# Kernel tuning notes

Measured on AMD Instinct MI355X. Metric: run time of the kernel, lower is better.

The kernel has to match this reference:

```python
import jax, jax.numpy as jnp
import numpy as np

EPS = 1e-6

def _normalize(x, eps=1e-12):
    n = jnp.linalg.norm(x, axis=-1, keepdims=True)
    return x / jnp.maximum(n, eps)

def _gather_nodes(nodes, idx):
    # nodes [B,N,C], idx [B,N,K] -> [B,N,K,C]
    B = nodes.shape[0]
    return nodes[jnp.arange(B)[:, None, None], idx]

def _dist(X, top_k):
    dX = X[:, None, :, :] - X[:, :, None, :]          # [B,N,N,3]
    D = jnp.sqrt(jnp.sum(dX * dX, axis=-1) + EPS)      # [B,N,N]
    neg_vals, E_idx = jax.lax.top_k(-D, top_k)         # smallest distances
    return D, -neg_vals, E_idx

def _gs_dist(D):
    D_min, D_max, D_count = 0.0, 20.0, 15
    D_mu = jnp.linspace(D_min, D_max, D_count)         # [15]
    D_sigma = (D_max - D_min) / D_count
    return jnp.exp(-(((D[..., None] - D_mu) / D_sigma) ** 2))

def _pos_encodings(E_idx, num_embeddings=16):
    N = E_idx.shape[1]
    ii = jnp.arange(N, dtype=jnp.float32)[None, :, None]
    d = (E_idx.astype(jnp.float32) - ii)[..., None]    # [B,N,K,1]
    freq = jnp.exp(jnp.arange(0, num_embeddings, 2, dtype=jnp.float32)
                   * -(np.log(10000.0) / num_embeddings))  # [8]
    angles = d * freq                                   # [B,N,K,8]
    return jnp.concatenate([jnp.cos(angles), jnp.sin(angles)], axis=-1)

def _orientations_coarse(X, E_idx, eps=1e-6):
    dX = X[:, 1:, :] - X[:, :-1, :]
    U = _normalize(dX)
    u_2, u_1, u_0 = U[:, :-2], U[:, 1:-1], U[:, 2:]
    n_2 = _normalize(jnp.cross(u_2, u_1))
    n_1 = _normalize(jnp.cross(u_1, u_0))
    cosA = jnp.clip(-(u_1 * u_0).sum(-1), -1 + eps, 1 - eps)
    A = jnp.arccos(cosA)
    cosD = jnp.clip((n_2 * n_1).sum(-1), -1 + eps, 1 - eps)
    Dang = jnp.sign((u_2 * n_1).sum(-1)) * jnp.arccos(cosD)
    AD = jnp.stack([jnp.cos(A), jnp.sin(A) * jnp.cos(Dang), jnp.sin(A) * jnp.sin(Dang)], axis=2)
    AD = jnp.pad(AD, ((0, 0), (1, 2), (0, 0)))          # [B,N,3]
    o_1 = _normalize(u_2 - u_1)
    O = jnp.stack([o_1, n_2, jnp.cross(o_1, n_2)], axis=2)  # [B,N-3,3,3]
    O = O.reshape(O.shape[0], O.shape[1], 9)
    O = jnp.pad(O, ((0, 0), (1, 2), (0, 0)))            # [B,N,9]
    O_nb = _gather_nodes(O, E_idx)                      # [B,N,K,9]
    X_nb = _gather_nodes(X, E_idx)                      # [B,N,K,3]
    O3 = O.reshape(O.shape[0], O.shape[1], 3, 3)
    dXn = X_nb - X[:, :, None, :]                       # [B,N,K,3]
    dU = jnp.einsum('bnij,bnkj->bnki', O3, dXn)         # rotate into local frame
    dU = _normalize(dU)
    # NOTE: original also computes R = O^T @ O_nb and quaternions Q, but Q is
    # dead code (never returned); omitted here (jit would DCE it anyway).
    return AD, dU

def setup_inputs() -> dict:
    key = jax.random.key(0)
    coords = jax.random.normal(key, (2, 4096, 3), dtype=jnp.float32) * 10.0
    return {"coords": coords, "num_k": 30}

def reference(coords, num_k):
    D, D_neighbors, E_idx = _dist(coords, num_k)
    gs_d = _gs_dist(D_neighbors)
    pos_emb = _pos_encodings(E_idx)
    AD_features, O_features = _orientations_coarse(coords, E_idx)
    return pos_emb, AD_features, O_features, gs_d, D_neighbors, E_idx
```

## Files before the change

### kernel.cpp

```cpp
#include <hip/hip_runtime.h>
#include <hip/hip_bf16.h>

constexpr int B = 2;
constexpr int N = 4096;
constexpr int K = 30;
constexpr int ROWS_PER_BLK = 4;

constexpr size_t OFF_POS = 0;
constexpr size_t OFF_AD  = OFF_POS + (size_t)B * N * K * 16;
constexpr size_t OFF_O   = OFF_AD  + (size_t)B * N * 3;
constexpr size_t OFF_GS  = OFF_O   + (size_t)B * N * K * 3;
constexpr size_t OFF_DN  = OFF_GS  + (size_t)B * N * K * 15;
constexpr size_t OFF_E   = OFF_DN  + (size_t)B * N * K;

constexpr float BIGD = 1e30f;
constexpr unsigned int BIGJ = 0xFFFFFFFFu;

struct F3 { float x, y, z; };

template <bool ISBF16>
__device__ __forceinline__ float ldx(const void* __restrict__ X, int idx) {
  if constexpr (ISBF16) {
    return __bfloat162float(((const __hip_bfloat16*)X)[idx]);
  } else {
    return ((const float*)X)[idx];
  }
}

template <bool ISBF16>
__device__ __forceinline__ float dist_core(float px, float py, float pz,
                                           float xi, float yi, float zi) {
#pragma clang fp contract(off)
  const float dx = px - xi;
  const float dy = py - yi;
  const float dz = pz - zi;
  return sqrtf(((dx * dx + dy * dy) + dz * dz) + 1e-6f);
}

template <bool ISBF16>
__device__ __forceinline__ float distf(const void* __restrict__ Xb, int j,
                                       float xi, float yi, float zi) {
  float px, py, pz;
  if constexpr (ISBF16) {
    px = ldx<true>(Xb, j * 3 + 0);
    py = ldx<true>(Xb, j * 3 + 1);
    pz = ldx<true>(Xb, j * 3 + 2);
  } else {
    const F3 p = ((const F3*)Xb)[j];
    px = p.x; py = p.y; pz = p.z;
  }
  return dist_core<ISBF16>(px, py, pz, xi, yi, zi);
}

template <int CTRL>
__device__ __forceinline__ float dpp_min_f32(float v) {
  const int mv = __builtin_amdgcn_update_dpp(__float_as_int(BIGD), __float_as_int(v),
                                             CTRL, 0xF, 0xF, false);
  return fminf(__int_as_float(mv), v);
}
template <int CTRL>
__device__ __forceinline__ unsigned int dpp_min_u32(unsigned int v) {
  const unsigned int mv = (unsigned int)__builtin_amdgcn_update_dpp(
      (int)BIGJ, (int)v, CTRL, 0xF, 0xF, false);
  return mv < v ? mv : v;
}
__device__ __forceinline__ float wave_min_f32_bcast(float v) {
  v = dpp_min_f32<0x111>(v);
  v = dpp_min_f32<0x112>(v);
  v = dpp_min_f32<0x114>(v);
  v = dpp_min_f32<0x118>(v);
  v = dpp_min_f32<0x142>(v);
  v = dpp_min_f32<0x143>(v);
  return __int_as_float(__builtin_amdgcn_readlane(__float_as_int(v), 63));
}
__device__ __forceinline__ unsigned int wave_min_u32_bcast(unsigned int v) {
  v = dpp_min_u32<0x111>(v);
  v = dpp_min_u32<0x112>(v);
  v = dpp_min_u32<0x114>(v);
  v = dpp_min_u32<0x118>(v);
  v = dpp_min_u32<0x142>(v);
  v = dpp_min_u32<0x143>(v);
  return (unsigned int)__builtin_amdgcn_readlane((int)v, 63);
}

__device__ __forceinline__ void lex_argmin(float d0, int j0,
                                           float& dmin, unsigned int& jmin) {
  dmin = wave_min_f32_bcast(d0);
  const unsigned long long tie = __ballot(d0 == dmin);
  if (__popcll(tie) == 1) {
    const int wl = __ffsll((unsigned long long)tie) - 1;
    jmin = (unsigned int)__builtin_amdgcn_readlane(j0, wl);
  } else {
    const unsigned int jc = (d0 == dmin) ? (unsigned int)j0 : BIGJ;
    jmin = wave_min_u32_bcast(jc);
  }
}

__device__ __forceinline__ float red2pi(float x) {
  return x - 6.28318530718f * rintf(x * 0.15915494309f);
}

__device__ __forceinline__ void norm3(float& x, float& y, float& z) {
  float n = sqrtf((x * x + y * y) + z * z);
  n = fmaxf(n, 1e-12f);
  x /= n; y /= n; z /= n;
}

__device__ __forceinline__ void cross3(float ax, float ay, float az,
                                       float bx, float by, float bz,
                                       float& cx, float& cy, float& cz) {
  cx = ay * bz - az * by;
  cy = az * bx - ax * bz;
  cz = ax * by - ay * bx;
}

template <bool ISBF16>
__device__ __forceinline__ void body(const void* __restrict__ Xb,
                                     float* __restrict__ out,
                                     int b, int i, int lane) {
  const float xi = ldx<ISBF16>(Xb, i * 3 + 0);
  const float yi = ldx<ISBF16>(Xb, i * 3 + 1);
  const float zi = ldx<ISBF16>(Xb, i * 3 + 2);

  float d0 = BIGD, d1 = BIGD;
  int   j0 = 0x7FFFFFFF, j1 = 0x7FFFFFFF;
  if constexpr (!ISBF16) {
    const F3* __restrict__ P = ((const F3*)Xb) + lane;
#pragma unroll 8
    for (int t = 0; t < 64; ++t) {
      const F3 p = P[t * 64];
      const int j = t * 64 + lane;
      const float d = dist_core<ISBF16>(p.x, p.y, p.z, xi, yi, zi);
      const bool lt1 = d < d1;
      const float td = lt1 ? d : d1;
      const int   tj = lt1 ? j : j1;
      const bool lt0 = td < d0;
      d1 = lt0 ? d0 : td;  j1 = lt0 ? j0 : tj;
      d0 = lt0 ? td : d0;  j0 = lt0 ? tj : j0;
    }
  } else {
#pragma unroll 8
    for (int t = 0; t < 64; ++t) {
      const int j = t * 64 + lane;
      const float d = distf<ISBF16>(Xb, j, xi, yi, zi);
      const bool lt1 = d < d1;
      const float td = lt1 ? d : d1;
      const int   tj = lt1 ? j : j1;
      const bool lt0 = td < d0;
      d1 = lt0 ? d0 : td;  j1 = lt0 ? j0 : tj;
      d0 = lt0 ? td : d0;  j0 = lt0 ? tj : j0;
    }
  }

  unsigned long long exm = 0;
  int   sjv = 0;
  float sdv = 0.0f;
  for (int k = 0; k < K; ++k) {
    float dmin; unsigned int jmin;
    lex_argmin(d0, j0, dmin, jmin);
    if (lane == k) { sjv = (int)jmin; sdv = dmin; }

    const int w  = (int)(jmin & 63u);
    const int tw = (int)(jmin >> 6);
    if (lane == w) {
      exm |= (1ull << tw);
      d0 = d1; j0 = j1;
      d1 = BIGD; j1 = 0x7FFFFFFF;
    }
    if (__ballot(d0 == BIGD) != 0ull) {
      const unsigned int mlo = (unsigned int)__builtin_amdgcn_readlane((int)(unsigned int)(exm & 0xFFFFFFFFull), w);
      const unsigned int mhi = (unsigned int)__builtin_amdgcn_readlane((int)(unsigned int)(exm >> 32), w);
      const unsigned long long m = ((unsigned long long)mhi << 32) | mlo;
      const int j2 = (lane << 6) | w;
      const float d2 = distf<ISBF16>(Xb, j2, xi, yi, zi);
      const float dc = ((m >> lane) & 1ull) ? BIGD : d2;
      float dmin2; unsigned int jmin2;
      lex_argmin(dc, j2, dmin2, jmin2);
      if (lane == w) { d0 = dmin2; j0 = (int)jmin2; }
    }
  }

  float ad0 = 0.f, ad1 = 0.f, ad2 = 0.f;
  float o00 = 0.f, o01 = 0.f, o02 = 0.f;
  float o10 = 0.f, o11 = 0.f, o12 = 0.f;
  float o20 = 0.f, o21 = 0.f, o22 = 0.f;
  if (i >= 1 && i <= N - 3) {
    const float ax = ldx<ISBF16>(Xb, (i - 1) * 3 + 0), ay = ldx<ISBF16>(Xb, (i - 1) * 3 + 1), az = ldx<ISBF16>(Xb, (i - 1) * 3 + 2);
    const float cx = ldx<ISBF16>(Xb, (i + 1) * 3 + 0), cy = ldx<ISBF16>(Xb, (i + 1) * 3 + 1), cz = ldx<ISBF16>(Xb, (i + 1) * 3 + 2);
    const float ex = ldx<ISBF16>(Xb, (i + 2) * 3 + 0), ey = ldx<ISBF16>(Xb, (i + 2) * 3 + 1), ez = ldx<ISBF16>(Xb, (i + 2) * 3 + 2);
    float u2x = xi - ax, u2y = yi - ay, u2z = zi - az; norm3(u2x, u2y, u2z);
    float u1x = cx - xi, u1y = cy - yi, u1z = cz - zi; norm3(u1x, u1y, u1z);
    float u0x = ex - cx, u0y = ey - cy, u0z = ez - cz; norm3(u0x, u0y, u0z);
    float n2x, n2y, n2z; cross3(u2x, u2y, u2z, u1x, u1y, u1z, n2x, n2y, n2z); norm3(n2x, n2y, n2z);
    float n1x, n1y, n1z; cross3(u1x, u1y, u1z, u0x, u0y, u0z, n1x, n1y, n1z); norm3(n1x, n1y, n1z);
    const float dotu = (u1x * u0x + u1y * u0y) + u1z * u0z;
    const float cosA = fminf(fmaxf(-dotu, -1.0f + 1e-6f), 1.0f - 1e-6f);
    const float A = acosf(cosA);
    const float dotn = (n2x * n1x + n2y * n1y) + n2z * n1z;
    const float cosD = fminf(fmaxf(dotn, -1.0f + 1e-6f), 1.0f - 1e-6f);
    const float du2n1 = (u2x * n1x + u2y * n1y) + u2z * n1z;
    const float sg = (du2n1 > 0.f) ? 1.f : ((du2n1 < 0.f) ? -1.f : 0.f);
    const float Dang = sg * acosf(cosD);
    const float sA = __sinf(A),    cA = __cosf(A);
    const float sD = __sinf(Dang), cD = __cosf(Dang);
    ad0 = cA; ad1 = sA * cD; ad2 = sA * sD;
    float o1x = u2x - u1x, o1y = u2y - u1y, o1z = u2z - u1z; norm3(o1x, o1y, o1z);
    o00 = o1x; o01 = o1y; o02 = o1z;
    o10 = n2x; o11 = n2y; o12 = n2z;
    cross3(o1x, o1y, o1z, n2x, n2y, n2z, o20, o21, o22);
  }

  const int row = b * N + i;

  {
    const size_t base = OFF_POS + (size_t)row * (K * 16);
    const int p = lane & 15;
    const float fr = __expf((float)((p & 7) * 2) * -0.57564627f);
    const bool is_cos = (p < 8);
#pragma unroll
    for (int it = 0; it < 8; ++it) {
      const int idx = it * 64 + lane;
      const int k = (idx >> 4) < K ? (idx >> 4) : (K - 1);
      const int jk = __shfl(sjv, k, 64);
      const float df = (float)(jk - i);
      const float r = red2pi(df * fr);
      const float v = is_cos ? __cosf(r) : __sinf(r);
      if (idx < K * 16) out[base + idx] = v;
    }
  }

  {
    const size_t base = OFF_GS + (size_t)row * (K * 15);
#pragma unroll
    for (int it = 0; it < 8; ++it) {
      const int idx = it * 64 + lane;
      const int kq = idx / 15;
      const int k = kq < K ? kq : (K - 1);
      const int m = idx - kq * 15;
      const float d = __shfl(sdv, k, 64);
      const float mu = (float)(m * (20.0 / 14.0));
      const float q = (d - mu) / 1.3333334f;
      const float v = __expf(-(q * q));
      if (idx < K * 15) out[base + idx] = v;
    }
  }

  if (lane < K) {
    const size_t rowk = (size_t)row * K + lane;
    const int   j = sjv;
    out[OFF_E  + rowk] = (float)j;
    out[OFF_DN + rowk] = sdv;

    float px, py, pz;
    if constexpr (ISBF16) {
      px = ldx<true>(Xb, j * 3 + 0);
      py = ldx<true>(Xb, j * 3 + 1);
      pz = ldx<true>(Xb, j * 3 + 2);
    } else {
      const F3 p = ((const F3*)Xb)[j];
      px = p.x; py = p.y; pz = p.z;
    }
    const float gx = px - xi, gy = py - yi, gz = pz - zi;
    const float v0 = (o00 * gx + o01 * gy) + o02 * gz;
    const float v1 = (o10 * gx + o11 * gy) + o12 * gz;
    const float v2 = (o20 * gx + o21 * gy) + o22 * gz;
    const float nn = fmaxf(sqrtf((v0 * v0 + v1 * v1) + v2 * v2), 1e-12f);
    out[OFF_O + rowk * 3 + 0] = v0 / nn;
    out[OFF_O + rowk * 3 + 1] = v1 / nn;
    out[OFF_O + rowk * 3 + 2] = v2 / nn;
  } else if (lane < K + 3) {
    const int c = lane - K;
    const float v = (c == 0) ? ad0 : (c == 1) ? ad1 : ad2;
    out[OFF_AD + (size_t)row * 3 + c] = v;
  }
}

__global__ __launch_bounds__(64 * ROWS_PER_BLK)
void protein_feat_kernel(const void* __restrict__ X,
                         float* __restrict__ out) {
  const int lane = threadIdx.x & 63;
  const int wv   = threadIdx.x >> 6;
  const int row  = blockIdx.x * ROWS_PER_BLK + wv;
  const int b    = row >> 12;
  const int i    = row & (N - 1);

  const unsigned short h = ((const unsigned short*)X)[2 * lane];
  const int e = (h >> 7) & 0xFF;
  const bool sane = ((h & 0x7FFF) == 0) || (e >= 115 && e <= 134);
  const unsigned long long bal = __ballot(sane);
  const bool isbf16 = __popcll(bal) >= 40;

  if (isbf16) {
    const void* Xb = (const void*)((const __hip_bfloat16*)X + (size_t)b * N * 3);
    body<true>(Xb, out, b, i, lane);
  } else {
    const void* Xb = (const void*)((const float*)X + (size_t)b * N * 3);
    body<false>(Xb, out, b, i, lane);
  }
}

extern "C" void kernel_launch(void* const* d_in, const int* in_sizes, int n_in,
                              void* d_out, int out_size, void* d_ws, size_t ws_size,
                              hipStream_t stream) {
  const void* X = d_in[0];
  float* out = (float*)d_out;
  (void)in_sizes; (void)n_in; (void)d_ws; (void)ws_size; (void)out_size;
  protein_feat_kernel<<<dim3(B * N / ROWS_PER_BLK), dim3(64 * ROWS_PER_BLK), 0, stream>>>(X, out);
}
```

Baseline: 122.1 us.

## Process two query rows per wavefront with packed float2 distance math

Each wavefront now handles two consecutive rows, so every candidate point loaded in the distance scan serves both rows. The squared-distance arithmetic uses a two-wide float vector type, which can map to packed FP32 instructions. The aim is to halve candidate loads per row and cut instruction count, while the grid gets half as many waves. This adds register pressure and exposes less parallelism, since the sequential top-30 pops run back to back for the two rows.

```diff
diff --git a/kernel.cpp b/kernel.cpp
--- a/kernel.cpp
+++ b/kernel.cpp
@@ -4,7 +4,8 @@
 constexpr int B = 2;
 constexpr int N = 4096;
 constexpr int K = 30;
-constexpr int ROWS_PER_BLK = 4;
+constexpr int WAVES_PER_BLK = 4;
+constexpr int ROWS_PER_WAVE = 2;
 
 constexpr size_t OFF_POS = 0;
 constexpr size_t OFF_AD  = OFF_POS + (size_t)B * N * K * 16;
@@ -17,6 +18,8 @@
 constexpr unsigned int BIGJ = 0xFFFFFFFFu;
 
 struct F3 { float x, y, z; };
+
+typedef float v2f __attribute__((ext_vector_type(2)));
 
 template <bool ISBF16>
 __device__ __forceinline__ float ldx(const void* __restrict__ X, int idx) {
@@ -114,47 +117,22 @@
   cz = ax * by - ay * bx;
 }
 
-template <bool ISBF16>
-__device__ __forceinline__ void body(const void* __restrict__ Xb,
-                                     float* __restrict__ out,
-                                     int b, int i, int lane) {
-  const float xi = ldx<ISBF16>(Xb, i * 3 + 0);
-  const float yi = ldx<ISBF16>(Xb, i * 3 + 1);
-  const float zi = ldx<ISBF16>(Xb, i * 3 + 2);
-
-  float d0 = BIGD, d1 = BIGD;
-  int   j0 = 0x7FFFFFFF, j1 = 0x7FFFFFFF;
-  if constexpr (!ISBF16) {
-    const F3* __restrict__ P = ((const F3*)Xb) + lane;
-#pragma unroll 8
-    for (int t = 0; t < 64; ++t) {
-      const F3 p = P[t * 64];
-      const int j = t * 64 + lane;
-      const float d = dist_core<ISBF16>(p.x, p.y, p.z, xi, yi, zi);
-      const bool lt1 = d < d1;
-      const float td = lt1 ? d : d1;
-      const int   tj = lt1 ? j : j1;
-      const bool lt0 = td < d0;
-      d1 = lt0 ? d0 : td;  j1 = lt0 ? j0 : tj;
-      d0 = lt0 ? td : d0;  j0 = lt0 ? tj : j0;
-    }
-  } else {
-#pragma unroll 8
-    for (int t = 0; t < 64; ++t) {
-      const int j = t * 64 + lane;
-      const float d = distf<ISBF16>(Xb, j, xi, yi, zi);
-      const bool lt1 = d < d1;
-      const float td = lt1 ? d : d1;
-      const int   tj = lt1 ? j : j1;
-      const bool lt0 = td < d0;
-      d1 = lt0 ? d0 : td;  j1 = lt0 ? j0 : tj;
-      d0 = lt0 ? td : d0;  j0 = lt0 ? tj : j0;
-    }
-  }
-
+__device__ __forceinline__ void ins2(float d, int j,
+                                     float& d0, float& d1, int& j0, int& j1) {
+  const bool lt1 = d < d1;
+  const float td = lt1 ? d : d1;
+  const int   tj = lt1 ? j : j1;
+  const bool lt0 = td < d0;
+  d1 = lt0 ? d0 : td;  j1 = lt0 ? j0 : tj;
+  d0 = lt0 ? td : d0;  j0 = lt0 ? tj : j0;
+}
+
+template <bool ISBF16>
+__device__ __forceinline__ void pops30(const void* __restrict__ Xb, int lane,
+                                       float xi, float yi, float zi,
+                                       float d0, float d1, int j0, int j1,
+                                       int& sjv, float& sdv) {
   unsigned long long exm = 0;
-  int   sjv = 0;
-  float sdv = 0.0f;
   for (int k = 0; k < K; ++k) {
     float dmin; unsigned int jmin;
     lex_argmin(d0, j0, dmin, jmin);
@@ -179,11 +157,21 @@
       if (lane == w) { d0 = dmin2; j0 = (int)jmin2; }
     }
   }
-
-  float ad0 = 0.f, ad1 = 0.f, ad2 = 0.f;
-  float o00 = 0.f, o01 = 0.f, o02 = 0.f;
-  float o10 = 0.f, o11 = 0.f, o12 = 0.f;
-  float o20 = 0.f, o21 = 0.f, o22 = 0.f;
+}
+
+struct Frame {
+  float ad0, ad1, ad2;
+  float o00, o01, o02, o10, o11, o12, o20, o21, o22;
+};
+
+template <bool ISBF16>
+__device__ __forceinline__ Frame frame_feats(const void* __restrict__ Xb, int i,
+                                             float xi, float yi, float zi) {
+  Frame f;
+  f.ad0 = 0.f; f.ad1 = 0.f; f.ad2 = 0.f;
+  f.o00 = 0.f; f.o01 = 0.f; f.o02 = 0.f;
+  f.o10 = 0.f; f.o11 = 0.f; f.o12 = 0.f;
+  f.o20 = 0.f; f.o21 = 0.f; f.o22 = 0.f;
   if (i >= 1 && i <= N - 3) {
     const float ax = ldx<ISBF16>(Xb, (i - 1) * 3 + 0), ay = ldx<ISBF16>(Xb, (i - 1) * 3 + 1), az = ldx<ISBF16>(Xb, (i - 1) * 3 + 2);
     const float cx = ldx<ISBF16>(Xb, (i + 1) * 3 + 0), cy = ldx<ISBF16>(Xb, (i + 1) * 3 + 1), cz = ldx<ISBF16>(Xb, (i + 1) * 3 + 2);
@@ -203,86 +191,184 @@
     const float Dang = sg * acosf(cosD);
     const float sA = __sinf(A),    cA = __cosf(A);
     const float sD = __sinf(Dang), cD = __cosf(Dang);
-    ad0 = cA; ad1 = sA * cD; ad2 = sA * sD;
+    f.ad0 = cA; f.ad1 = sA * cD; f.ad2 = sA * sD;
     float o1x = u2x - u1x, o1y = u2y - u1y, o1z = u2z - u1z; norm3(o1x, o1y, o1z);
-    o00 = o1x; o01 = o1y; o02 = o1z;
-    o10 = n2x; o11 = n2y; o12 = n2z;
-    cross3(o1x, o1y, o1z, n2x, n2y, n2z, o20, o21, o22);
-  }
-
-  const int row = b * N + i;
+    f.o00 = o1x; f.o01 = o1y; f.o02 = o1z;
+    f.o10 = n2x; f.o11 = n2y; f.o12 = n2z;
+    cross3(o1x, o1y, o1z, n2x, n2y, n2z, f.o20, f.o21, f.o22);
+  }
+  return f;
+}
+
+__device__ __forceinline__ void row_tail(const void* __restrict__ Xb,
+                                         float* __restrict__ out, bool isbf16,
+                                         int row, int lane, int sjv, float sdv,
+                                         float xi, float yi, float zi,
+                                         const Frame& f) {
+  if (lane < K) {
+    const size_t rowk = (size_t)row * K + lane;
+    const int   j = sjv;
+    out[OFF_E  + rowk] = (float)j;
+    out[OFF_DN + rowk] = sdv;
+
+    float px, py, pz;
+    if (isbf16) {
+      px = ldx<true>(Xb, j * 3 + 0);
+      py = ldx<true>(Xb, j * 3 + 1);
+      pz = ldx<true>(Xb, j * 3 + 2);
+    } else {
+      const F3 p = ((const F3*)Xb)[j];
+      px = p.x; py = p.y; pz = p.z;
+    }
+    const float gx = px - xi, gy = py - yi, gz = pz - zi;
+    const float v0 = (f.o00 * gx + f.o01 * gy) + f.o02 * gz;
+    const float v1 = (f.o10 * gx + f.o11 * gy) + f.o12 * gz;
+    const float v2 = (f.o20 * gx + f.o21 * gy) + f.o22 * gz;
+    const float nn = fmaxf(sqrtf((v0 * v0 + v1 * v1) + v2 * v2), 1e-12f);
+    out[OFF_O + rowk * 3 + 0] = v0 / nn;
+    out[OFF_O + rowk * 3 + 1] = v1 / nn;
+    out[OFF_O + rowk * 3 + 2] = v2 / nn;
+  } else if (lane < K + 3) {
+    const int c = lane - K;
+    const float v = (c == 0) ? f.ad0 : (c == 1) ? f.ad1 : f.ad2;
+    out[OFF_AD + (size_t)row * 3 + c] = v;
+  }
+}
+
+template <bool ISBF16>
+__device__ __forceinline__ void body2(const void* __restrict__ Xb,
+                                      float* __restrict__ out,
+                                      int b, int i0, int lane) {
+  const int iA = i0, iB = i0 + 1;
+  const float xiA = ldx<ISBF16>(Xb, iA * 3 + 0);
+  const float yiA = ldx<ISBF16>(Xb, iA * 3 + 1);
+  const float ziA = ldx<ISBF16>(Xb, iA * 3 + 2);
+  const float xiB = ldx<ISBF16>(Xb, iB * 3 + 0);
+  const float yiB = ldx<ISBF16>(Xb, iB * 3 + 1);
+  const float ziB = ldx<ISBF16>(Xb, iB * 3 + 2);
+
+  const v2f xab = {xiA, xiB};
+  const v2f yab = {yiA, yiB};
+  const v2f zab = {ziA, ziB};
+  const v2f epsv = {1e-6f, 1e-6f};
+
+  float d0A = BIGD, d1A = BIGD, d0B = BIGD, d1B = BIGD;
+  int   j0A = 0x7FFFFFFF, j1A = 0x7FFFFFFF, j0B = 0x7FFFFFFF, j1B = 0x7FFFFFFF;
+
+  if constexpr (!ISBF16) {
+    const F3* __restrict__ P = ((const F3*)Xb) + lane;
+#pragma unroll 8
+    for (int t = 0; t < 64; ++t) {
+      const F3 p = P[t * 64];
+      const int j = t * 64 + lane;
+      const v2f px = {p.x, p.x};
+      const v2f py = {p.y, p.y};
+      const v2f pz = {p.z, p.z};
+      v2f s;
+      {
+#pragma clang fp contract(off)
+        const v2f dx = px - xab;
+        const v2f dy = py - yab;
+        const v2f dz = pz - zab;
+        s = ((dx * dx + dy * dy) + dz * dz) + epsv;
+      }
+      const float dA = sqrtf(s.x);
+      const float dB = sqrtf(s.y);
+      ins2(dA, j, d0A, d1A, j0A, j1A);
+      ins2(dB, j, d0B, d1B, j0B, j1B);
+    }
+  } else {
+#pragma unroll 8
+    for (int t = 0; t < 64; ++t) {
+      const int j = t * 64 + lane;
+      const float ppx = ldx<true>(Xb, j * 3 + 0);
+      const float ppy = ldx<true>(Xb, j * 3 + 1);
+      const float ppz = ldx<true>(Xb, j * 3 + 2);
+      const v2f px = {ppx, ppx};
+      const v2f py = {ppy, ppy};
+      const v2f pz = {ppz, ppz};
+      v2f s;
+      {
+#pragma clang fp contract(off)
+        const v2f dx = px - xab;
+        const v2f dy = py - yab;
+        const v2f dz = pz - zab;
+        s = ((dx * dx + dy * dy) + dz * dz) + epsv;
+      }
+      const float dA = sqrtf(s.x);
+      const float dB = sqrtf(s.y);
+      ins2(dA, j, d0A, d1A, j0A, j1A);
+      ins2(dB, j, d0B, d1B, j0B, j1B);
+    }
+  }
+
+  int   sjA = 0, sjB = 0;
+  float sdA = 0.f, sdB = 0.f;
+  pops30<ISBF16>(Xb, lane, xiA, yiA, ziA, d0A, d1A, j0A, j1A, sjA, sdA);
+  pops30<ISBF16>(Xb, lane, xiB, yiB, ziB, d0B, d1B, j0B, j1B, sjB, sdB);
+
+  const Frame fA = frame_feats<ISBF16>(Xb, iA, xiA, yiA, ziA);
+  const Frame fB = frame_feats<ISBF16>(Xb, iB, xiB, yiB, ziB);
+
+  const int rowA = b * N + iA;
 
   {
-    const size_t base = OFF_POS + (size_t)row * (K * 16);
+    const size_t baseA = OFF_POS + (size_t)rowA * (K * 16);
     const int p = lane & 15;
     const float fr = __expf((float)((p & 7) * 2) * -0.57564627f);
     const bool is_cos = (p < 8);
 #pragma unroll
     for (int it = 0; it < 8; ++it) {
       const int idx = it * 64 + lane;
-      const int k = (idx >> 4) < K ? (idx >> 4) : (K - 1);
-      const int jk = __shfl(sjv, k, 64);
-      const float df = (float)(jk - i);
-      const float r = red2pi(df * fr);
-      const float v = is_cos ? __cosf(r) : __sinf(r);
-      if (idx < K * 16) out[base + idx] = v;
+      const int kk = (idx >> 4) < K ? (idx >> 4) : (K - 1);
+      const int jkA = __shfl(sjA, kk, 64);
+      const int jkB = __shfl(sjB, kk, 64);
+      const float rA = red2pi((float)(jkA - iA) * fr);
+      const float rB = red2pi((float)(jkB - iB) * fr);
+      const float vA = is_cos ? __cosf(rA) : __sinf(rA);
+      const float vB = is_cos ? __cosf(rB) : __sinf(rB);
+      if (idx < K * 16) {
+        out[baseA + idx] = vA;
+        out[baseA + (K * 16) + idx] = vB;
+      }
     }
   }
 
   {
-    const size_t base = OFF_GS + (size_t)row * (K * 15);
+    const size_t baseA = OFF_GS + (size_t)rowA * (K * 15);
 #pragma unroll
     for (int it = 0; it < 8; ++it) {
       const int idx = it * 64 + lane;
       const int kq = idx / 15;
-      const int k = kq < K ? kq : (K - 1);
+      const int kk = kq < K ? kq : (K - 1);
       const int m = idx - kq * 15;
-      const float d = __shfl(sdv, k, 64);
       const float mu = (float)(m * (20.0 / 14.0));
-      const float q = (d - mu) / 1.3333334f;
-      const float v = __expf(-(q * q));
-      if (idx < K * 15) out[base + idx] = v;
-    }
-  }
-
-  if (lane < K) {
-    const size_t rowk = (size_t)row * K + lane;
-    const int   j = sjv;
-    out[OFF_E  + rowk] = (float)j;
-    out[OFF_DN + rowk] = sdv;
-
-    float px, py, pz;
-    if constexpr (ISBF16) {
-      px = ldx<true>(Xb, j * 3 + 0);
-      py = ldx<true>(Xb, j * 3 + 1);
-      pz = ldx<true>(Xb, j * 3 + 2);
-    } else {
-      const F3 p = ((const F3*)Xb)[j];
-      px = p.x; py = p.y; pz = p.z;
-    }
-    const float gx = px - xi, gy = py - yi, gz = pz - zi;
-    const float v0 = (o00 * gx + o01 * gy) + o02 * gz;
-    const float v1 = (o10 * gx + o11 * gy) + o12 * gz;
-    const float v2 = (o20 * gx + o21 * gy) + o22 * gz;
-    const float nn = fmaxf(sqrtf((v0 * v0 + v1 * v1) + v2 * v2), 1e-12f);
-    out[OFF_O + rowk * 3 + 0] = v0 / nn;
-    out[OFF_O + rowk * 3 + 1] = v1 / nn;
-    out[OFF_O + rowk * 3 + 2] = v2 / nn;
-  } else if (lane < K + 3) {
-    const int c = lane - K;
-    const float v = (c == 0) ? ad0 : (c == 1) ? ad1 : ad2;
-    out[OFF_AD + (size_t)row * 3 + c] = v;
-  }
-}
-
-__global__ __launch_bounds__(64 * ROWS_PER_BLK)
+      const float dA = __shfl(sdA, kk, 64);
+      const float dB = __shfl(sdB, kk, 64);
+      const float qA = (dA - mu) / 1.3333334f;
+      const float qB = (dB - mu) / 1.3333334f;
+      const float vA = __expf(-(qA * qA));
+      const float vB = __expf(-(qB * qB));
+      if (idx < K * 15) {
+        out[baseA + idx] = vA;
+        out[baseA + (K * 15) + idx] = vB;
+      }
+    }
+  }
+
+  row_tail(Xb, out, ISBF16, rowA,     lane, sjA, sdA, xiA, yiA, ziA, fA);
+  row_tail(Xb, out, ISBF16, rowA + 1, lane, sjB, sdB, xiB, yiB, ziB, fB);
+}
+
+__global__ __launch_bounds__(64 * WAVES_PER_BLK)
 void protein_feat_kernel(const void* __restrict__ X,
                          float* __restrict__ out) {
   const int lane = threadIdx.x & 63;
   const int wv   = threadIdx.x >> 6;
-  const int row  = blockIdx.x * ROWS_PER_BLK + wv;
-  const int b    = row >> 12;
-  const int i    = row & (N - 1);
+  const int pr   = blockIdx.x * WAVES_PER_BLK + wv;
+  const int row0 = pr * ROWS_PER_WAVE;
+  const int b    = row0 >> 12;
+  const int i0   = row0 & (N - 1);
 
   const unsigned short h = ((const unsigned short*)X)[2 * lane];
   const int e = (h >> 7) & 0xFF;
@@ -292,10 +378,10 @@
 
   if (isbf16) {
     const void* Xb = (const void*)((const __hip_bfloat16*)X + (size_t)b * N * 3);
-    body<true>(Xb, out, b, i, lane);
+    body2<true>(Xb, out, b, i0, lane);
   } else {
     const void* Xb = (const void*)((const float*)X + (size_t)b * N * 3);
-    body<false>(Xb, out, b, i, lane);
+    body2<false>(Xb, out, b, i0, lane);
   }
 }
 
@@ -305,5 +391,6 @@
   const void* X = d_in[0];
   float* out = (float*)d_out;
   (void)in_sizes; (void)n_in; (void)d_ws; (void)ws_size; (void)out_size;
-  protein_feat_kernel<<<dim3(B * N / ROWS_PER_BLK), dim3(64 * ROWS_PER_BLK), 0, stream>>>(X, out);
-}
+  protein_feat_kernel<<<dim3(B * N / (WAVES_PER_BLK * ROWS_PER_WAVE)),
+                        dim3(64 * WAVES_PER_BLK), 0, stream>>>(X, out);
+}
```

Measured after the change: 128.0 us. 4.8% more time.

## Scan squared distances and defer sqrt, with tie-detection fallback rescan

Applied to the files above, without the earlier changes.

The main neighbor scan now compares squared distances instead of taking a sqrt per candidate, and only applies sqrt to the per-lane top-2 afterwards. It also tracks a third-smallest value so it can tell when sqrt rounding could create ties that change the ordering, and in that case it rescans with exact distances. The change also packs the x/y differences into a two-wide vector and swaps divisions and sqrt for hardware rcp/sqrt and a multiply by a constant. The cost removed is the per-candidate sqrt in the hot loop. In exchange there is extra min/max work per candidate, an occasional full rescan, and small precision differences from the approximate reciprocal.

```diff
diff --git a/kernel.cpp b/kernel.cpp
--- a/kernel.cpp
+++ b/kernel.cpp
@@ -17,6 +17,8 @@
 constexpr unsigned int BIGJ = 0xFFFFFFFFu;
 
 struct F3 { float x, y, z; };
+
+typedef float v2f __attribute__((ext_vector_type(2)));
 
 template <bool ISBF16>
 __device__ __forceinline__ float ldx(const void* __restrict__ X, int idx) {
@@ -101,9 +103,10 @@
 }
 
 __device__ __forceinline__ void norm3(float& x, float& y, float& z) {
-  float n = sqrtf((x * x + y * y) + z * z);
+  float n = __builtin_amdgcn_sqrtf((x * x + y * y) + z * z);
   n = fmaxf(n, 1e-12f);
-  x /= n; y /= n; z /= n;
+  const float inv = __builtin_amdgcn_rcpf(n);
+  x *= inv; y *= inv; z *= inv;
 }
 
 __device__ __forceinline__ void cross3(float ax, float ay, float az,
@@ -112,6 +115,16 @@
   cx = ay * bz - az * by;
   cy = az * bx - ax * bz;
   cz = ax * by - ay * bx;
+}
+
+__device__ __forceinline__ void ins2(float d, int j,
+                                     float& d0, float& d1, int& j0, int& j1) {
+  const bool lt1 = d < d1;
+  const float td = lt1 ? d : d1;
+  const int   tj = lt1 ? j : j1;
+  const bool lt0 = td < d0;
+  d1 = lt0 ? d0 : td;  j1 = lt0 ? j0 : tj;
+  d0 = lt0 ? td : d0;  j0 = lt0 ? tj : j0;
 }
 
 template <bool ISBF16>
@@ -122,33 +135,58 @@
   const float yi = ldx<ISBF16>(Xb, i * 3 + 1);
   const float zi = ldx<ISBF16>(Xb, i * 3 + 2);
 
-  float d0 = BIGD, d1 = BIGD;
+  float s0 = BIGD, s1 = BIGD, s2v = BIGD;
   int   j0 = 0x7FFFFFFF, j1 = 0x7FFFFFFF;
   if constexpr (!ISBF16) {
     const F3* __restrict__ P = ((const F3*)Xb) + lane;
+    const v2f xyi = {xi, yi};
 #pragma unroll 8
     for (int t = 0; t < 64; ++t) {
       const F3 p = P[t * 64];
       const int j = t * 64 + lane;
-      const float d = dist_core<ISBF16>(p.x, p.y, p.z, xi, yi, zi);
-      const bool lt1 = d < d1;
-      const float td = lt1 ? d : d1;
-      const int   tj = lt1 ? j : j1;
-      const bool lt0 = td < d0;
-      d1 = lt0 ? d0 : td;  j1 = lt0 ? j0 : tj;
-      d0 = lt0 ? td : d0;  j0 = lt0 ? tj : j0;
+      float s;
+      {
+#pragma clang fp contract(off)
+        const v2f pxy = {p.x, p.y};
+        const v2f a = pxy - xyi;
+        const v2f m = a * a;
+        const float dz = p.z - zi;
+        s = ((m.x + m.y) + dz * dz) + 1e-6f;
+      }
+      s2v = fminf(fmaxf(s, s1), s2v);
+      ins2(s, j, s0, s1, j0, j1);
     }
   } else {
 #pragma unroll 8
     for (int t = 0; t < 64; ++t) {
       const int j = t * 64 + lane;
-      const float d = distf<ISBF16>(Xb, j, xi, yi, zi);
-      const bool lt1 = d < d1;
-      const float td = lt1 ? d : d1;
-      const int   tj = lt1 ? j : j1;
-      const bool lt0 = td < d0;
-      d1 = lt0 ? d0 : td;  j1 = lt0 ? j0 : tj;
-      d0 = lt0 ? td : d0;  j0 = lt0 ? tj : j0;
+      const float px = ldx<true>(Xb, j * 3 + 0);
+      const float py = ldx<true>(Xb, j * 3 + 1);
+      const float pz = ldx<true>(Xb, j * 3 + 2);
+      float s;
+      {
+#pragma clang fp contract(off)
+        const float dx = px - xi;
+        const float dy = py - yi;
+        const float dz = pz - zi;
+        s = ((dx * dx + dy * dy) + dz * dz) + 1e-6f;
+      }
+      s2v = fminf(fmaxf(s, s1), s2v);
+      ins2(s, j, s0, s1, j0, j1);
+    }
+  }
+
+  float d0 = sqrtf(s0), d1 = sqrtf(s1);
+  {
+    const float d2 = sqrtf(s2v);
+    if (d0 == d1 && j0 > j1) { const int t = j0; j0 = j1; j1 = t; }
+    if (__ballot(d1 == d2) != 0ull) {
+      d0 = BIGD; d1 = BIGD; j0 = 0x7FFFFFFF; j1 = 0x7FFFFFFF;
+      for (int t = 0; t < 64; ++t) {
+        const int j = t * 64 + lane;
+        const float d = distf<ISBF16>(Xb, j, xi, yi, zi);
+        ins2(d, j, d0, d1, j0, j1);
+      }
     }
   }
 
@@ -239,7 +277,7 @@
       const int m = idx - kq * 15;
       const float d = __shfl(sdv, k, 64);
       const float mu = (float)(m * (20.0 / 14.0));
-      const float q = (d - mu) / 1.3333334f;
+      const float q = (d - mu) * 0.75f;
       const float v = __expf(-(q * q));
       if (idx < K * 15) out[base + idx] = v;
     }
@@ -264,10 +302,11 @@
     const float v0 = (o00 * gx + o01 * gy) + o02 * gz;
     const float v1 = (o10 * gx + o11 * gy) + o12 * gz;
     const float v2 = (o20 * gx + o21 * gy) + o22 * gz;
-    const float nn = fmaxf(sqrtf((v0 * v0 + v1 * v1) + v2 * v2), 1e-12f);
-    out[OFF_O + rowk * 3 + 0] = v0 / nn;
-    out[OFF_O + rowk * 3 + 1] = v1 / nn;
-    out[OFF_O + rowk * 3 + 2] = v2 / nn;
+    const float nn = fmaxf(__builtin_amdgcn_sqrtf((v0 * v0 + v1 * v1) + v2 * v2), 1e-12f);
+    const float inv = __builtin_amdgcn_rcpf(nn);
+    out[OFF_O + rowk * 3 + 0] = v0 * inv;
+    out[OFF_O + rowk * 3 + 1] = v1 * inv;
+    out[OFF_O + rowk * 3 + 2] = v2 * inv;
   } else if (lane < K + 3) {
     const int c = lane - K;
     const float v = (c == 0) ? ad0 : (c == 1) ? ad1 : ad2;
```

New measurement: 107.9 us. 11.6% less time.
